# Kernel optimization log

Measured on AMD Instinct MI355X. Metric: run time of the kernel, lower is better.

The kernel has to match this reference:

```python
import jax, jax.numpy as jnp
import numpy as np

B, S, H, D = 2, 4096, 16, 64


def setup_inputs() -> dict:
    key = jax.random.key(0)
    qkv = jax.random.normal(key, (B, S, 3, H, D), dtype=jnp.float32)
    return {"qkv": qkv}


def reference(qkv) -> jnp.ndarray:
    batch, seq_len, three, num_heads, head_dim = qkv.shape
    softmax_scale = head_dim ** (-0.5)
    q = qkv[:, :, 0]  # (B, S, H, D)
    k = qkv[:, :, 1]
    v = qkv[:, :, 2]
    # (B, H, S, S) score matrix, faithful to the naive matmul+mask+softmax path
    scores = jnp.einsum('bshd,bthd->bhst', q, k) * softmax_scale
    row = jnp.arange(seq_len)[:, None]
    col = jnp.arange(seq_len)[None, :]
    causal = row >= col  # (S, S) bool
    scores = jnp.where(causal[None, None, :, :], scores, -1000000000.0)
    attn = jax.nn.softmax(scores, axis=-1)
    out = jnp.einsum('bhst,bthd->bshd', attn, v)  # (B, S, H, D)
    return out
```

## Files before the change

kernel.cpp:

```cpp
#include <hip/hip_runtime.h>


#define S_LEN 4096
#define NHEAD 16
#define HDIM 64
#define QBLK 128
#define KVBLK 64
#define NQT (S_LEN / QBLK)
#define LDK 72
#define ROWSTRIDE (3 * NHEAD * HDIM)

using bf16x8 = __attribute__((ext_vector_type(8))) short;
using bf16x4 = __attribute__((ext_vector_type(4))) short;
using f32x4  = __attribute__((ext_vector_type(4))) float;

#define MFMA32(A, B, C) __builtin_amdgcn_mfma_f32_16x16x32_bf16((A), (B), (C), 0, 0, 0)
#define MFMA16(A, B, C) __builtin_amdgcn_mfma_f32_16x16x16bf16_1k((A), (B), (C), 0, 0, 0)

#if __has_builtin(__builtin_amdgcn_exp2f)
#define EXP2F(x) __builtin_amdgcn_exp2f(x)
#else
#define EXP2F(x) exp2f(x)
#endif

__device__ __forceinline__ int f2bf2(float lo, float hi) {
  int r;
  asm("v_cvt_pk_bf16_f32 %0, %1, %2" : "=v"(r) : "v"(lo), "v"(hi));
  return r;
}

__global__ __launch_bounds__(256, 2)
void attn_fwd(const float* __restrict__ qkv, float* __restrict__ out) {
  __shared__ short Ks[KVBLK][LDK] __attribute__((aligned(16)));
  __shared__ short VTs[HDIM][LDK] __attribute__((aligned(16)));

  const int flat = (int)blockIdx.x + 32 * (int)blockIdx.y;
  const int u    = flat & 255;
  const int j    = flat >> 8;
  const int bh   = u >> 3;
  const int t8   = u & 7;
  const int qt   = (j == 0) ? t8 : (j == 1) ? 31 - t8 : (j == 2) ? 8 + t8 : 23 - t8;

  const int b    = bh >> 4;
  const int h    = bh & 15;
  const int tid  = threadIdx.x;
  const int wid  = tid >> 6;
  const int lane = tid & 63;
  const int lq   = lane & 15;
  const int lg   = lane >> 4;

  const float* basep = qkv + (size_t)b * S_LEN * ROWSTRIDE + h * HDIM;
  const float* kbase = basep + NHEAD * HDIM;
  const float* vbase = basep + 2 * NHEAD * HDIM;

  const int rb = (tid >> 4) * 4;
  const int cb = (tid & 15) * 4;

  f32x4 kreg[4], vreg[4];
  auto load_tile = [&](int kvt) {
    const int kr = kvt * KVBLK + rb;
#pragma unroll
    for (int i = 0; i < 4; ++i) {
      kreg[i] = *reinterpret_cast<const f32x4*>(kbase + (size_t)(kr + i) * ROWSTRIDE + cb);
      vreg[i] = *reinterpret_cast<const f32x4*>(vbase + (size_t)(kr + i) * ROWSTRIDE + cb);
    }
  };
  auto store_tile = [&]() {
#pragma unroll
    for (int i = 0; i < 4; ++i) {
      union { bf16x4 v; int w[2]; } kk;
      kk.w[0] = f2bf2(kreg[i][0], kreg[i][1]);
      kk.w[1] = f2bf2(kreg[i][2], kreg[i][3]);
      *reinterpret_cast<bf16x4*>(&Ks[rb + i][cb]) = kk.v;
    }
#pragma unroll
    for (int e = 0; e < 4; ++e) {
      union { bf16x4 v; int w[2]; } vv;
      vv.w[0] = f2bf2(vreg[0][e], vreg[1][e]);
      vv.w[1] = f2bf2(vreg[2][e], vreg[3][e]);
      *reinterpret_cast<bf16x4*>(&VTs[cb + e][rb]) = vv.v;
    }
  };

  const float SC = 0.18033688011112042f;

  const int wq = qt * QBLK + wid * 32;

  bf16x8 qf[2][2];
#pragma unroll
  for (int rt = 0; rt < 2; ++rt) {
    const float* qp = basep + (size_t)(wq + rt * 16 + lq) * ROWSTRIDE + 8 * lg;
#pragma unroll
    for (int t = 0; t < 2; ++t) {
      f32x4 x0 = *reinterpret_cast<const f32x4*>(qp + 32 * t);
      f32x4 x1 = *reinterpret_cast<const f32x4*>(qp + 32 * t + 4);
      union { bf16x8 v; int w[4]; } uq;
      uq.w[0] = f2bf2(x0[0] * SC, x0[1] * SC);
      uq.w[1] = f2bf2(x0[2] * SC, x0[3] * SC);
      uq.w[2] = f2bf2(x1[0] * SC, x1[1] * SC);
      uq.w[3] = f2bf2(x1[2] * SC, x1[3] * SC);
      qf[rt][t] = uq.v;
    }
  }

  f32x4 acc[2][4];
#pragma unroll
  for (int rt = 0; rt < 2; ++rt)
#pragma unroll
    for (int dt = 0; dt < 4; ++dt)
      acc[rt][dt] = (f32x4){0.f, 0.f, 0.f, 0.f};

  float mrun[2] = {-1e30f, -1e30f};
  float lrun[2] = {0.f, 0.f};

  const int nkv = 2 * qt + 2;
  load_tile(0);

  for (int kvt = 0; kvt < nkv; ++kvt) {
    __syncthreads();
    store_tile();
    __syncthreads();
    if (kvt + 1 < nkv) load_tile(kvt + 1);

    const int kvb = kvt * KVBLK;
    if (kvb > wq + 31) continue;

    f32x4 sc[2][4];
#pragma unroll
    for (int rt = 0; rt < 2; ++rt)
#pragma unroll
      for (int c = 0; c < 4; ++c)
        sc[rt][c] = (f32x4){0.f, 0.f, 0.f, 0.f};

#pragma unroll
    for (int c = 0; c < 4; ++c) {
      bf16x8 k0 = *reinterpret_cast<const bf16x8*>(&Ks[c * 16 + lq][8 * lg]);
      bf16x8 k1 = *reinterpret_cast<const bf16x8*>(&Ks[c * 16 + lq][8 * lg + 32]);
#pragma unroll
      for (int rt = 0; rt < 2; ++rt) {
        sc[rt][c] = MFMA32(k0, qf[rt][0], sc[rt][c]);
        sc[rt][c] = MFMA32(k1, qf[rt][1], sc[rt][c]);
      }
    }

    if (kvb + KVBLK - 1 > wq) {
#pragma unroll
      for (int rt = 0; rt < 2; ++rt) {
        const int q0 = wq + rt * 16 + lq;
#pragma unroll
        for (int c = 0; c < 4; ++c)
#pragma unroll
          for (int r = 0; r < 4; ++r)
            if (kvb + c * 16 + 4 * lg + r > q0) sc[rt][c][r] = -1e30f;
      }
    }

    bf16x4 pf[2][4];
    float alpha[2];
#pragma unroll
    for (int rt = 0; rt < 2; ++rt) {
      float c0 = fmaxf(fmaxf(sc[rt][0][0], sc[rt][0][1]), fmaxf(sc[rt][0][2], sc[rt][0][3]));
      float c1 = fmaxf(fmaxf(sc[rt][1][0], sc[rt][1][1]), fmaxf(sc[rt][1][2], sc[rt][1][3]));
      float c2 = fmaxf(fmaxf(sc[rt][2][0], sc[rt][2][1]), fmaxf(sc[rt][2][2], sc[rt][2][3]));
      float c3 = fmaxf(fmaxf(sc[rt][3][0], sc[rt][3][1]), fmaxf(sc[rt][3][2], sc[rt][3][3]));
      float tm = fmaxf(fmaxf(c0, c1), fmaxf(c2, c3));
      tm = fmaxf(tm, __shfl_xor(tm, 16));
      tm = fmaxf(tm, __shfl_xor(tm, 32));
      const float newm = fmaxf(mrun[rt], tm);
      alpha[rt] = EXP2F(mrun[rt] - newm);
      mrun[rt] = newm;

      float ts = 0.f;
#pragma unroll
      for (int c = 0; c < 4; ++c) {
        float p0 = EXP2F(sc[rt][c][0] - newm);
        float p1 = EXP2F(sc[rt][c][1] - newm);
        float p2 = EXP2F(sc[rt][c][2] - newm);
        float p3 = EXP2F(sc[rt][c][3] - newm);
        ts += (p0 + p1) + (p2 + p3);
        union { bf16x4 v; int w[2]; } pp;
        pp.w[0] = f2bf2(p0, p1);
        pp.w[1] = f2bf2(p2, p3);
        pf[rt][c] = pp.v;
      }
      ts += __shfl_xor(ts, 16);
      ts += __shfl_xor(ts, 32);
      lrun[rt] = lrun[rt] * alpha[rt] + ts;
    }

#pragma unroll
    for (int rt = 0; rt < 2; ++rt) {
      const float a0 = __shfl(alpha[rt], 4 * lg + 0);
      const float a1 = __shfl(alpha[rt], 4 * lg + 1);
      const float a2 = __shfl(alpha[rt], 4 * lg + 2);
      const float a3 = __shfl(alpha[rt], 4 * lg + 3);
#pragma unroll
      for (int dt = 0; dt < 4; ++dt) {
        acc[rt][dt][0] *= a0;
        acc[rt][dt][1] *= a1;
        acc[rt][dt][2] *= a2;
        acc[rt][dt][3] *= a3;
      }
    }

#pragma unroll
    for (int dt = 0; dt < 4; ++dt) {
#pragma unroll
      for (int c = 0; c < 4; ++c) {
        bf16x4 vf = *reinterpret_cast<const bf16x4*>(&VTs[dt * 16 + lq][c * 16 + 4 * lg]);
        acc[0][dt] = MFMA16(pf[0][c], vf, acc[0][dt]);
        acc[1][dt] = MFMA16(pf[1][c], vf, acc[1][dt]);
      }
    }
  }

#pragma unroll
  for (int rt = 0; rt < 2; ++rt) {
    const float l0 = __shfl(lrun[rt], 4 * lg + 0);
    const float l1 = __shfl(lrun[rt], 4 * lg + 1);
    const float l2 = __shfl(lrun[rt], 4 * lg + 2);
    const float l3 = __shfl(lrun[rt], 4 * lg + 3);
    const f32x4 linv = {1.f / l0, 1.f / l1, 1.f / l2, 1.f / l3};
#pragma unroll
    for (int dt = 0; dt < 4; ++dt) {
#pragma unroll
      for (int r = 0; r < 4; ++r) {
        out[(size_t)(b * S_LEN + wq + rt * 16 + 4 * lg + r) * (NHEAD * HDIM) + h * HDIM + dt * 16 + lq] =
            acc[rt][dt][r] * linv[r];
      }
    }
  }
}

extern "C" void kernel_launch(void* const* d_in, const int* in_sizes, int n_in,
                              void* d_out, int out_size, void* d_ws, size_t ws_size,
                              hipStream_t stream) {
  const float* qkv = (const float*)d_in[0];
  float* o = (float*)d_out;
  dim3 grid(NQT, 2 * NHEAD);
  attn_fwd<<<grid, 256, 0, stream>>>(qkv, o);
}
```

Before: 177.2 us.

## Prefetch two KV tiles ahead, swizzle V^T smem, add setprio and max3

Double-buffers the K/V register tiles so global loads are issued two tiles ahead, giving more time to hide HBM latency. The transposed V tile in shared memory gets an XOR swizzle on its column index to reduce LDS bank conflicts on both the store and the MFMA operand reads. It also raises wave priority around the MFMA sections and uses v_max3 for the row-max reduction. The extra register buffer raises VGPR pressure, which could limit the two-blocks-per-CU occupancy target.

After: 190.4 us. 7.5% more time.

```diff
diff --git a/kernel.cpp b/kernel.cpp
--- a/kernel.cpp
+++ b/kernel.cpp
@@ -29,6 +29,12 @@
   return r;
 }
 
+__device__ __forceinline__ float max3f(float a, float b, float c) {
+  float d;
+  asm("v_max3_f32 %0, %1, %2, %3" : "=v"(d) : "v"(a), "v"(b), "v"(c));
+  return d;
+}
+
 __global__ __launch_bounds__(256, 2)
 void attn_fwd(const float* __restrict__ qkv, float* __restrict__ out) {
   __shared__ short Ks[KVBLK][LDK] __attribute__((aligned(16)));
@@ -55,9 +61,9 @@
 
   const int rb = (tid >> 4) * 4;
   const int cb = (tid & 15) * 4;
-
-  f32x4 kreg[4], vreg[4];
-  auto load_tile = [&](int kvt) {
+  const int vcol = 4 * ((rb >> 2) ^ (cb >> 3));
+
+  auto load_tile = [&](int kvt, f32x4 (&kreg)[4], f32x4 (&vreg)[4]) {
     const int kr = kvt * KVBLK + rb;
 #pragma unroll
     for (int i = 0; i < 4; ++i) {
@@ -65,7 +71,7 @@
       vreg[i] = *reinterpret_cast<const f32x4*>(vbase + (size_t)(kr + i) * ROWSTRIDE + cb);
     }
   };
-  auto store_tile = [&]() {
+  auto store_tile = [&](const f32x4 (&kreg)[4], const f32x4 (&vreg)[4]) {
 #pragma unroll
     for (int i = 0; i < 4; ++i) {
       union { bf16x4 v; int w[2]; } kk;
@@ -78,7 +84,7 @@
       union { bf16x4 v; int w[2]; } vv;
       vv.w[0] = f2bf2(vreg[0][e], vreg[1][e]);
       vv.w[1] = f2bf2(vreg[2][e], vreg[3][e]);
-      *reinterpret_cast<bf16x4*>(&VTs[cb + e][rb]) = vv.v;
+      *reinterpret_cast<bf16x4*>(&VTs[cb + e][vcol]) = vv.v;
     }
   };
 
@@ -114,104 +120,119 @@
   float lrun[2] = {0.f, 0.f};
 
   const int nkv = 2 * qt + 2;
-  load_tile(0);
-
-  for (int kvt = 0; kvt < nkv; ++kvt) {
+
+  auto step = [&](int kvt, f32x4 (&kreg)[4], f32x4 (&vreg)[4]) {
     __syncthreads();
-    store_tile();
+    store_tile(kreg, vreg);
     __syncthreads();
-    if (kvt + 1 < nkv) load_tile(kvt + 1);
+    if (kvt + 2 < nkv) load_tile(kvt + 2, kreg, vreg);
 
     const int kvb = kvt * KVBLK;
-    if (kvb > wq + 31) continue;
-
-    f32x4 sc[2][4];
-#pragma unroll
-    for (int rt = 0; rt < 2; ++rt)
-#pragma unroll
-      for (int c = 0; c < 4; ++c)
-        sc[rt][c] = (f32x4){0.f, 0.f, 0.f, 0.f};
-
-#pragma unroll
-    for (int c = 0; c < 4; ++c) {
-      bf16x8 k0 = *reinterpret_cast<const bf16x8*>(&Ks[c * 16 + lq][8 * lg]);
-      bf16x8 k1 = *reinterpret_cast<const bf16x8*>(&Ks[c * 16 + lq][8 * lg + 32]);
+    if (kvb <= wq + 31) {
+      f32x4 sc[2][4];
+#pragma unroll
+      for (int rt = 0; rt < 2; ++rt)
+#pragma unroll
+        for (int c = 0; c < 4; ++c)
+          sc[rt][c] = (f32x4){0.f, 0.f, 0.f, 0.f};
+
+      __builtin_amdgcn_s_setprio(1);
+#pragma unroll
+      for (int c = 0; c < 4; ++c) {
+        bf16x8 k0 = *reinterpret_cast<const bf16x8*>(&Ks[c * 16 + lq][8 * lg]);
+        bf16x8 k1 = *reinterpret_cast<const bf16x8*>(&Ks[c * 16 + lq][8 * lg + 32]);
+#pragma unroll
+        for (int rt = 0; rt < 2; ++rt) {
+          sc[rt][c] = MFMA32(k0, qf[rt][0], sc[rt][c]);
+          sc[rt][c] = MFMA32(k1, qf[rt][1], sc[rt][c]);
+        }
+      }
+      __builtin_amdgcn_s_setprio(0);
+
+      if (kvb + KVBLK - 1 > wq) {
+#pragma unroll
+        for (int rt = 0; rt < 2; ++rt) {
+          const int q0 = wq + rt * 16 + lq;
+#pragma unroll
+          for (int c = 0; c < 4; ++c)
+#pragma unroll
+            for (int r = 0; r < 4; ++r)
+              if (kvb + c * 16 + 4 * lg + r > q0) sc[rt][c][r] = -1e30f;
+        }
+      }
+
+      bf16x4 pf[2][4];
+      float alpha[2];
 #pragma unroll
       for (int rt = 0; rt < 2; ++rt) {
-        sc[rt][c] = MFMA32(k0, qf[rt][0], sc[rt][c]);
-        sc[rt][c] = MFMA32(k1, qf[rt][1], sc[rt][c]);
-      }
-    }
-
-    if (kvb + KVBLK - 1 > wq) {
+        float v0 = max3f(sc[rt][0][0], sc[rt][0][1], sc[rt][0][2]);
+        float v1 = max3f(sc[rt][0][3], sc[rt][1][0], sc[rt][1][1]);
+        float v2 = max3f(sc[rt][1][2], sc[rt][1][3], sc[rt][2][0]);
+        float v3 = max3f(sc[rt][2][1], sc[rt][2][2], sc[rt][2][3]);
+        float v4 = max3f(sc[rt][3][0], sc[rt][3][1], sc[rt][3][2]);
+        float tm = fmaxf(max3f(v0, v1, v2), max3f(v3, v4, sc[rt][3][3]));
+        tm = fmaxf(tm, __shfl_xor(tm, 16));
+        tm = fmaxf(tm, __shfl_xor(tm, 32));
+        const float newm = fmaxf(mrun[rt], tm);
+        alpha[rt] = EXP2F(mrun[rt] - newm);
+        mrun[rt] = newm;
+
+        float ts = 0.f;
+#pragma unroll
+        for (int c = 0; c < 4; ++c) {
+          float p0 = EXP2F(sc[rt][c][0] - newm);
+          float p1 = EXP2F(sc[rt][c][1] - newm);
+          float p2 = EXP2F(sc[rt][c][2] - newm);
+          float p3 = EXP2F(sc[rt][c][3] - newm);
+          ts += (p0 + p1) + (p2 + p3);
+          union { bf16x4 v; int w[2]; } pp;
+          pp.w[0] = f2bf2(p0, p1);
+          pp.w[1] = f2bf2(p2, p3);
+          pf[rt][c] = pp.v;
+        }
+        ts += __shfl_xor(ts, 16);
+        ts += __shfl_xor(ts, 32);
+        lrun[rt] = lrun[rt] * alpha[rt] + ts;
+      }
+
 #pragma unroll
       for (int rt = 0; rt < 2; ++rt) {
-        const int q0 = wq + rt * 16 + lq;
-#pragma unroll
-        for (int c = 0; c < 4; ++c)
-#pragma unroll
-          for (int r = 0; r < 4; ++r)
-            if (kvb + c * 16 + 4 * lg + r > q0) sc[rt][c][r] = -1e30f;
-      }
-    }
-
-    bf16x4 pf[2][4];
-    float alpha[2];
-#pragma unroll
-    for (int rt = 0; rt < 2; ++rt) {
-      float c0 = fmaxf(fmaxf(sc[rt][0][0], sc[rt][0][1]), fmaxf(sc[rt][0][2], sc[rt][0][3]));
-      float c1 = fmaxf(fmaxf(sc[rt][1][0], sc[rt][1][1]), fmaxf(sc[rt][1][2], sc[rt][1][3]));
-      float c2 = fmaxf(fmaxf(sc[rt][2][0], sc[rt][2][1]), fmaxf(sc[rt][2][2], sc[rt][2][3]));
-      float c3 = fmaxf(fmaxf(sc[rt][3][0], sc[rt][3][1]), fmaxf(sc[rt][3][2], sc[rt][3][3]));
-      float tm = fmaxf(fmaxf(c0, c1), fmaxf(c2, c3));
-      tm = fmaxf(tm, __shfl_xor(tm, 16));
-      tm = fmaxf(tm, __shfl_xor(tm, 32));
-      const float newm = fmaxf(mrun[rt], tm);
-      alpha[rt] = EXP2F(mrun[rt] - newm);
-      mrun[rt] = newm;
-
-      float ts = 0.f;
-#pragma unroll
-      for (int c = 0; c < 4; ++c) {
-        float p0 = EXP2F(sc[rt][c][0] - newm);
-        float p1 = EXP2F(sc[rt][c][1] - newm);
-        float p2 = EXP2F(sc[rt][c][2] - newm);
-        float p3 = EXP2F(sc[rt][c][3] - newm);
-        ts += (p0 + p1) + (p2 + p3);
-        union { bf16x4 v; int w[2]; } pp;
-        pp.w[0] = f2bf2(p0, p1);
-        pp.w[1] = f2bf2(p2, p3);
-        pf[rt][c] = pp.v;
-      }
-      ts += __shfl_xor(ts, 16);
-      ts += __shfl_xor(ts, 32);
-      lrun[rt] = lrun[rt] * alpha[rt] + ts;
-    }
-
-#pragma unroll
-    for (int rt = 0; rt < 2; ++rt) {
-      const float a0 = __shfl(alpha[rt], 4 * lg + 0);
-      const float a1 = __shfl(alpha[rt], 4 * lg + 1);
-      const float a2 = __shfl(alpha[rt], 4 * lg + 2);
-      const float a3 = __shfl(alpha[rt], 4 * lg + 3);
+        const float a0 = __shfl(alpha[rt], 4 * lg + 0);
+        const float a1 = __shfl(alpha[rt], 4 * lg + 1);
+        const float a2 = __shfl(alpha[rt], 4 * lg + 2);
+        const float a3 = __shfl(alpha[rt], 4 * lg + 3);
+#pragma unroll
+        for (int dt = 0; dt < 4; ++dt) {
+          acc[rt][dt][0] *= a0;
+          acc[rt][dt][1] *= a1;
+          acc[rt][dt][2] *= a2;
+          acc[rt][dt][3] *= a3;
+        }
+      }
+
+      __builtin_amdgcn_s_setprio(1);
 #pragma unroll
       for (int dt = 0; dt < 4; ++dt) {
-        acc[rt][dt][0] *= a0;
-        acc[rt][dt][1] *= a1;
-        acc[rt][dt][2] *= a2;
-        acc[rt][dt][3] *= a3;
-      }
-    }
-
-#pragma unroll
-    for (int dt = 0; dt < 4; ++dt) {
-#pragma unroll
-      for (int c = 0; c < 4; ++c) {
-        bf16x4 vf = *reinterpret_cast<const bf16x4*>(&VTs[dt * 16 + lq][c * 16 + 4 * lg]);
-        acc[0][dt] = MFMA16(pf[0][c], vf, acc[0][dt]);
-        acc[1][dt] = MFMA16(pf[1][c], vf, acc[1][dt]);
-      }
-    }
+        const int f = (2 * dt + (lq >> 3)) & 7;
+#pragma unroll
+        for (int c = 0; c < 4; ++c) {
+          bf16x4 vf = *reinterpret_cast<const bf16x4*>(&VTs[dt * 16 + lq][4 * ((4 * c + lg) ^ f)]);
+          acc[0][dt] = MFMA16(pf[0][c], vf, acc[0][dt]);
+          acc[1][dt] = MFMA16(pf[1][c], vf, acc[1][dt]);
+        }
+      }
+      __builtin_amdgcn_s_setprio(0);
+    }
+  };
+
+  f32x4 kA[4], vA[4], kB[4], vB[4];
+  load_tile(0, kA, vA);
+  load_tile(1, kB, vB);
+
+#pragma unroll 1
+  for (int kvt = 0; kvt < nkv; kvt += 2) {
+    step(kvt, kA, vA);
+    step(kvt + 1, kB, vB);
   }
 
 #pragma unroll
```
